# Kernel tuning notes

Measured on AMD Instinct MI355X. Metric: run time of the kernel, lower is better.

Reference implementation:

```python
import jax, jax.numpy as jnp
import numpy as np
from jax import lax

B = 32768        # batch
L = 1024         # input_size
K = 5            # kernel_size
PAD = K - 1      # circular padding = 4
FEA = L + (PAD - K // 2) * 2   # mem_fea_dim = 1028
MEM_DIM = 50
DATE_DIM = 32
SHRINK = 0.0025
EPS = 1e-12
DN = ('NCH', 'OIH', 'NCH')


def setup_inputs() -> dict:
    key = jax.random.key(0)
    ks = jax.random.split(key, 10)
    s = 0.05
    return {
        'x': jax.random.normal(ks[0], (B, L), jnp.float32),
        'date_vector': jax.random.normal(ks[1], (B, DATE_DIM), jnp.float32),
        'conv_w': jax.random.normal(ks[2], (1, 1, K), jnp.float32) * s,    # Conv1d weight [out,in,k]
        'convt_w': jax.random.normal(ks[3], (1, 1, K), jnp.float32) * s,   # ConvTranspose1d weight
        'mem_W': jax.random.normal(ks[4], (MEM_DIM, FEA), jnp.float32) * s,      # memory bank (codebook)
        'date_W': jax.random.normal(ks[5], (MEM_DIM, DATE_DIM), jnp.float32) * s, # date addressing weights
        'fcw_w': jax.random.normal(ks[6], (1, L), jnp.float32) * s,
        'fcw_b': jnp.zeros((1,), jnp.float32),
        'fcb_w': jax.random.normal(ks[7], (1, L), jnp.float32) * s,
        'fcb_b': jnp.zeros((1,), jnp.float32),
    }


def _forward(x, date_vector, conv_w, convt_w, mem_W, date_W, fcw_w, fcw_b, fcb_w, fcb_b):
    # --- encode: 1-channel circular conv (bias forced to 0 in original forward) ---
    st = x[:, None, :]                                            # [B,1,L]
    stp = jnp.pad(st, ((0, 0), (0, 0), (PAD, PAD)), mode='wrap')  # circular pad
    st = lax.conv_general_dilated(stp, conv_w, (1,), 'VALID', dimension_numbers=DN)  # [B,1,FEA]

    # --- DateMemoryUnit: date-addressed read with hard shrink + L1 renorm ---
    scores = date_vector @ date_W.T                               # [B,MEM_DIM]
    att = jax.nn.softmax(scores, axis=-1)
    att = jax.nn.relu(att - SHRINK) * att / (jnp.abs(att - SHRINK) + EPS)
    att = att / (jnp.sum(jnp.abs(att), axis=-1, keepdims=True) + EPS)
    st_mem = att @ mem_W                                          # [B,FEA]
    st = st_mem.reshape(B, 1, FEA)

    # --- decode: ConvTranspose1d(k=5, stride=1, padding=4) == VALID conv with flipped kernel ---
    st = lax.conv_general_dilated(st, jnp.flip(convt_w, -1), (1,), 'VALID', dimension_numbers=DN)
    st = st[:, 0, :]                                              # [B,L]

    # --- trend blend ---
    mtf = 0.5
    weight = jnp.tanh(x @ fcw_w.T + fcw_b) * mtf + 1.0            # [B,1]
    bias = jnp.tanh(x @ fcb_w.T + fcb_b) * mtf                    # [B,1]
    st = st * weight + bias
    return st, weight, bias


def reference(x, date_vector, conv_w, convt_w, mem_W, date_W, fcw_w, fcw_b, fcb_w, fcb_b):
    return _forward(x, date_vector, conv_w, convt_w, mem_W, date_W, fcw_w, fcw_b, fcb_w, fcb_b)
```

## Files before the change

kernel.cpp:

```cpp
#include <hip/hip_runtime.h>
#include <hip/hip_bf16.h>

#define BB   32768
#define LL   1024
#define FEA  1028
#define MEM  50
#define DATE 32

typedef float  f32x4  __attribute__((ext_vector_type(4)));
typedef __bf16 bf16x8 __attribute__((ext_vector_type(8)));

__device__ __forceinline__ float wave_max(float v) {
    #pragma unroll
    for (int off = 32; off; off >>= 1) v = fmaxf(v, __shfl_xor(v, off));
    return v;
}
__device__ __forceinline__ float wave_sum(float v) {
    #pragma unroll
    for (int off = 32; off; off >>= 1) v += __shfl_xor(v, off);
    return v;
}
__device__ __forceinline__ float fast_tanh(float v) {
    float e = __expf(2.f * v);
    return 1.f - 2.f / (e + 1.f);
}

__global__ __launch_bounds__(256) void prep_and_wb(
        const float* __restrict__ convt_w,
        const float* __restrict__ mem_W,
        const float* __restrict__ x,
        const float* __restrict__ fcw_w, const float* __restrict__ fcw_b,
        const float* __restrict__ fcb_w, const float* __restrict__ fcb_b,
        const float* __restrict__ dv,
        const float* __restrict__ dW,
        __bf16* __restrict__ wc,
        __bf16* __restrict__ att_g,
        float* __restrict__ out) {
    const int lane = threadIdx.x & 63;
    const int wid  = threadIdx.x >> 6;

    if (blockIdx.x >= 4096) {
        int idx = (blockIdx.x - 4096) * 256 + threadIdx.x;
        int n = idx >> 6, k = idx & 63;
        float acc = 0.f;
        if (k < MEM) {
            #pragma unroll
            for (int j = 0; j < 5; ++j)
                acc += convt_w[j] * mem_W[k * FEA + n + 4 - j];
        }
        wc[n * 64 + k] = (__bf16)acc;
        return;
    }

    if (blockIdx.x >= 2048) {
        const int b0 = (blockIdx.x - 2048) * 16;
        int m = lane < MEM ? lane : MEM - 1;
        float dwv[DATE];
        const f32x4* dwp = (const f32x4*)(dW + m * DATE);
        #pragma unroll
        for (int c = 0; c < 8; ++c) {
            f32x4 v = dwp[c];
            #pragma unroll
            for (int j = 0; j < 4; ++j) dwv[c * 4 + j] = v[j];
        }
        #pragma unroll
        for (int rr = 0; rr < 4; ++rr) {
            int r = b0 + wid * 4 + rr;
            const f32x4* dvp = (const f32x4*)(dv + (size_t)r * DATE);
            float sc = 0.f;
            #pragma unroll
            for (int c = 0; c < 8; ++c) {
                f32x4 v = dvp[c];
                #pragma unroll
                for (int j = 0; j < 4; ++j) sc += v[j] * dwv[c * 4 + j];
            }
            float scm = (lane < MEM) ? sc : -1e30f;
            float mx  = wave_max(scm);
            float e   = (lane < MEM) ? __expf(sc - mx) : 0.f;
            float s   = wave_sum(e);
            float p   = e / s;
            float d   = p - 0.0025f;
            float p2  = (d > 0.f) ? p * d / (d + 1e-12f) : 0.f;
            float s2  = wave_sum(p2) + 1e-12f;
            float att = p2 / s2;
            att_g[(size_t)r * 64 + lane] = (lane < MEM) ? (__bf16)att : (__bf16)0.f;
        }
        return;
    }

    const int b0 = blockIdx.x * 16;
    f32x4 wv[4], bv[4];
    #pragma unroll
    for (int c = 0; c < 4; ++c) {
        wv[c] = *(const f32x4*)(fcw_w + c * 256 + lane * 4);
        bv[c] = *(const f32x4*)(fcb_w + c * 256 + lane * 4);
    }
    f32x4 xv[4][4];
    #pragma unroll
    for (int rr = 0; rr < 4; ++rr)
        #pragma unroll
        for (int c = 0; c < 4; ++c)
            xv[rr][c] = *(const f32x4*)(x + (size_t)(b0 + wid * 4 + rr) * LL
                                          + c * 256 + lane * 4);
    float fwb = fcw_b[0], fbb = fcb_b[0];
    #pragma unroll
    for (int rr = 0; rr < 4; ++rr) {
        int r = wid * 4 + rr;
        float aw = 0.f, ab = 0.f;
        #pragma unroll
        for (int c = 0; c < 4; ++c)
            #pragma unroll
            for (int j = 0; j < 4; ++j) {
                aw += xv[rr][c][j] * wv[c][j];
                ab += xv[rr][c][j] * bv[c][j];
            }
        #pragma unroll
        for (int off = 1; off <= 32; off <<= 1) {
            aw += __shfl_xor(aw, off);
            ab += __shfl_xor(ab, off);
        }
        if (lane == 0) {
            out[(size_t)BB * LL + (b0 + r)]      = fast_tanh(aw + fwb) * 0.5f + 1.0f;
            out[(size_t)BB * LL + BB + (b0 + r)] = fast_tanh(ab + fbb) * 0.5f;
        }
    }
}

__global__ __launch_bounds__(256) void memconv_stream(
        const __bf16* __restrict__ wc,
        const __bf16* __restrict__ att_g,
        const float* __restrict__ wb,
        float* __restrict__ out) {
    __shared__ float stage[4][16 * 72];

    const int lane = threadIdx.x & 63;
    const int wid  = threadIdx.x >> 6;
    const int cg   = lane & 15;
    const int kg   = lane >> 4;
    const int rg   = wid & 1;
    const int nh   = wid >> 1;
    const int r0   = blockIdx.x * 32 + rg * 16;
    const int n0   = nh * 512;

    bf16x8 bfr0 = *(const bf16x8*)(att_g + (size_t)(r0 + cg) * 64 + kg * 8);
    bf16x8 bfr1 = *(const bf16x8*)(att_g + (size_t)(r0 + cg) * 64 + 32 + kg * 8);

    float w_reg = wb[r0 + cg];
    float b_reg = wb[BB + r0 + cg];
    float wj[4], bj[4];
    #pragma unroll
    for (int j = 0; j < 4; ++j) {
        wj[j] = __shfl(w_reg, j * 4 + kg);
        bj[j] = __shfl(b_reg, j * 4 + kg);
    }

    float* st = stage[wid];
    #pragma unroll 2
    for (int R = 0; R < 8; ++R) {
        #pragma unroll
        for (int t = 0; t < 4; ++t) {
            int n = n0 + R * 64 + t * 16 + cg;
            bf16x8 a0 = *(const bf16x8*)(wc + n * 64 + kg * 8);
            bf16x8 a1 = *(const bf16x8*)(wc + n * 64 + 32 + kg * 8);
            f32x4 acc = {0.f, 0.f, 0.f, 0.f};
            acc = __builtin_amdgcn_mfma_f32_16x16x32_bf16(a0, bfr0, acc, 0, 0, 0);
            acc = __builtin_amdgcn_mfma_f32_16x16x32_bf16(a1, bfr1, acc, 0, 0, 0);
            *(f32x4*)(st + cg * 72 + t * 16 + kg * 4) = acc;
        }
        #pragma unroll
        for (int j = 0; j < 4; ++j) {
            int row = j * 4 + kg;
            int nl  = cg * 4;
            f32x4 v = *(const f32x4*)(st + row * 72 + nl);
            f32x4 o;
            #pragma unroll
            for (int k = 0; k < 4; ++k) o[k] = v[k] * wj[j] + bj[j];
            *(f32x4*)(out + (size_t)(r0 + row) * LL + n0 + R * 64 + nl) = o;
        }
    }
}

extern "C" void kernel_launch(void* const* d_in, const int* in_sizes, int n_in,
                              void* d_out, int out_size, void* d_ws, size_t ws_size,
                              hipStream_t stream) {
    const float* x     = (const float*)d_in[0];
    const float* dv    = (const float*)d_in[1];
    const float* convt = (const float*)d_in[3];
    const float* memW  = (const float*)d_in[4];
    const float* dateW = (const float*)d_in[5];
    const float* fcww  = (const float*)d_in[6];
    const float* fcwb  = (const float*)d_in[7];
    const float* fcbw  = (const float*)d_in[8];
    const float* fcbb  = (const float*)d_in[9];
    float* out = (float*)d_out;
    __bf16* wc    = (__bf16*)d_ws;
    __bf16* att_g = (__bf16*)d_ws + 65536;

    prep_and_wb   <<<4352, 256, 0, stream>>>(convt, memW, x, fcww, fcwb, fcbw, fcbb,
                                             dv, dateW, wc, att_g, out);
    memconv_stream<<<BB / 32, 256, 0, stream>>>(wc, att_g, out + (size_t)BB * LL, out);
}
```

Baseline: 284.7 us.

## Drop LDS staging and store MFMA results directly from registers

The memory-conv output kernel now computes all 16 MFMA tiles of a 256-column strip into registers, applies the per-row weight and bias, then issues all stores directly. This removes the shared-memory transpose staging and its shuffles. Each block handles 16 batch rows split across 4 waves, with occupancy hinted via launch bounds. The catch is that stores become 64-byte segments spread over 16 rows rather than wide row-contiguous writes, which could hurt write coalescing.

New measurement: 295.0 us. 1.04x slower.

```diff
diff --git a/kernel.cpp b/kernel.cpp
--- a/kernel.cpp
+++ b/kernel.cpp
@@ -126,58 +126,43 @@
     }
 }
 
-__global__ __launch_bounds__(256) void memconv_stream(
+__global__ __launch_bounds__(256, 4) void memconv_store(
         const __bf16* __restrict__ wc,
         const __bf16* __restrict__ att_g,
         const float* __restrict__ wb,
         float* __restrict__ out) {
-    __shared__ float stage[4][16 * 72];
-
     const int lane = threadIdx.x & 63;
     const int wid  = threadIdx.x >> 6;
     const int cg   = lane & 15;
     const int kg   = lane >> 4;
-    const int rg   = wid & 1;
-    const int nh   = wid >> 1;
-    const int r0   = blockIdx.x * 32 + rg * 16;
-    const int n0   = nh * 512;
+    const int b0   = blockIdx.x * 16;
+    const int n0   = wid * 256;
 
-    bf16x8 bfr0 = *(const bf16x8*)(att_g + (size_t)(r0 + cg) * 64 + kg * 8);
-    bf16x8 bfr1 = *(const bf16x8*)(att_g + (size_t)(r0 + cg) * 64 + 32 + kg * 8);
+    bf16x8 bfr0 = *(const bf16x8*)(att_g + (size_t)(b0 + cg) * 64 + kg * 8);
+    bf16x8 bfr1 = *(const bf16x8*)(att_g + (size_t)(b0 + cg) * 64 + 32 + kg * 8);
+    float w  = wb[b0 + cg];
+    float bi = wb[BB + b0 + cg];
 
-    float w_reg = wb[r0 + cg];
-    float b_reg = wb[BB + r0 + cg];
-    float wj[4], bj[4];
+    f32x4 acc[16];
     #pragma unroll
-    for (int j = 0; j < 4; ++j) {
-        wj[j] = __shfl(w_reg, j * 4 + kg);
-        bj[j] = __shfl(b_reg, j * 4 + kg);
+    for (int t = 0; t < 16; ++t) {
+        int n = n0 + t * 16 + cg;
+        bf16x8 a0 = *(const bf16x8*)(wc + n * 64 + kg * 8);
+        bf16x8 a1 = *(const bf16x8*)(wc + n * 64 + 32 + kg * 8);
+        f32x4 z = {0.f, 0.f, 0.f, 0.f};
+        z      = __builtin_amdgcn_mfma_f32_16x16x32_bf16(a0, bfr0, z, 0, 0, 0);
+        acc[t] = __builtin_amdgcn_mfma_f32_16x16x32_bf16(a1, bfr1, z, 0, 0, 0);
     }
-
-    float* st = stage[wid];
-    #pragma unroll 2
-    for (int R = 0; R < 8; ++R) {
+    #pragma unroll
+    for (int t = 0; t < 16; ++t) {
         #pragma unroll
-        for (int t = 0; t < 4; ++t) {
-            int n = n0 + R * 64 + t * 16 + cg;
-            bf16x8 a0 = *(const bf16x8*)(wc + n * 64 + kg * 8);
-            bf16x8 a1 = *(const bf16x8*)(wc + n * 64 + 32 + kg * 8);
-            f32x4 acc = {0.f, 0.f, 0.f, 0.f};
-            acc = __builtin_amdgcn_mfma_f32_16x16x32_bf16(a0, bfr0, acc, 0, 0, 0);
-            acc = __builtin_amdgcn_mfma_f32_16x16x32_bf16(a1, bfr1, acc, 0, 0, 0);
-            *(f32x4*)(st + cg * 72 + t * 16 + kg * 4) = acc;
-        }
-        #pragma unroll
-        for (int j = 0; j < 4; ++j) {
-            int row = j * 4 + kg;
-            int nl  = cg * 4;
-            f32x4 v = *(const f32x4*)(st + row * 72 + nl);
-            f32x4 o;
-            #pragma unroll
-            for (int k = 0; k < 4; ++k) o[k] = v[k] * wj[j] + bj[j];
-            *(f32x4*)(out + (size_t)(r0 + row) * LL + n0 + R * 64 + nl) = o;
-        }
+        for (int k = 0; k < 4; ++k) acc[t][k] = acc[t][k] * w + bi;
     }
+    __builtin_amdgcn_sched_barrier(0);
+    float* dst = out + (size_t)(b0 + cg) * LL + n0 + kg * 4;
+    #pragma unroll
+    for (int t = 0; t < 16; ++t)
+        *(f32x4*)(dst + t * 16) = acc[t];
 }
 
 extern "C" void kernel_launch(void* const* d_in, const int* in_sizes, int n_in,
@@ -196,7 +181,7 @@
     __bf16* wc    = (__bf16*)d_ws;
     __bf16* att_g = (__bf16*)d_ws + 65536;
 
-    prep_and_wb   <<<4352, 256, 0, stream>>>(convt, memW, x, fcww, fcwb, fcbw, fcbb,
-                                             dv, dateW, wc, att_g, out);
-    memconv_stream<<<BB / 32, 256, 0, stream>>>(wc, att_g, out + (size_t)BB * LL, out);
+    prep_and_wb  <<<4352, 256, 0, stream>>>(convt, memW, x, fcww, fcwb, fcbw, fcbb,
+                                            dv, dateW, wc, att_g, out);
+    memconv_store<<<BB / 16, 256, 0, stream>>>(wc, att_g, out + (size_t)BB * LL, out);
 }
```
